# Performance work log

Hardware: AMD Instinct MI355X
Metric: run time of the kernel (lower is better)

## Reference

```python
import jax, jax.numpy as jnp
import numpy as np

B, D, N = 256, 128, 65536
P, K, P2 = 100, 4096, 10
T, MOM = 0.07, 0.5


def setup_inputs() -> dict:
    key = jax.random.key(0)
    k1, k2, k3, k4, k5 = jax.random.split(key, 5)
    stdv = 1.0 / np.sqrt(D / 3.0)
    memory_v1 = jax.random.uniform(k1, (N, D), minval=-stdv, maxval=stdv, dtype=jnp.float32)
    memory_v2 = jax.random.uniform(k2, (N, D), minval=-stdv, maxval=stdv, dtype=jnp.float32)
    v1 = jax.random.normal(k3, (B, D), dtype=jnp.float32)
    v2 = jax.random.normal(k4, (B, D), dtype=jnp.float32)
    y = jnp.arange(B, dtype=jnp.int32)  # unique sample ids in the bank
    idx = jax.random.randint(k5, (B, K + P), 0, N, dtype=jnp.int32)
    idx = idx.at[:, 0].set(y)  # first column is the ground-truth positive (as in torch)
    return {"epoch": 0, "v1": v1, "v2": v2, "y": y, "idx": idx,
            "memory_v1": memory_v1, "memory_v2": memory_v2}


def reference(epoch, v1, v2, y, idx, memory_v1, memory_v2):
    # --- gather contrastive keys from the memory banks (detached in torch) ---
    w1 = jax.lax.stop_gradient(memory_v1)[idx]  # [B, K+P, D]
    w2 = jax.lax.stop_gradient(memory_v2)[idx]  # [B, K+P, D]

    # similarity logits against the student feature v2
    out = jnp.exp(jnp.einsum('bkd,bd->bk', w1, v2) / T)  # [B, K+P]

    # --- hard positive selection via teacher/student relation gap ---
    t_rel = jnp.einsum('bkd,bd->bk',
                       w1 / jnp.linalg.norm(w1, axis=2, keepdims=True),
                       v1 / jnp.linalg.norm(v1, axis=1, keepdims=True))
    s_rel = jnp.einsum('bkd,bd->bk',
                       w2 / jnp.linalg.norm(w2, axis=2, keepdims=True),
                       v2 / jnp.linalg.norm(v2, axis=1, keepdims=True))
    diff = t_rel[:, :P] - s_rel[:, :P]            # [B, P]
    order = jnp.argsort(-diff, axis=1)            # descending sort ('hard' mode)
    sel = order[:, :P2].at[:, 0].set(0)           # force slot 0 = ground-truth positive

    out_pos = jnp.take_along_axis(out, sel, axis=1)  # [B, P2]
    out_neg = out[:, P:P + K]                        # [B, K]
    out_cat = jnp.concatenate([out_pos, out_neg], axis=1)  # [B, P2+K]

    # normalization constant Z (first-iteration estimate; a detached scalar in torch)
    Z = jax.lax.stop_gradient(out_cat.mean() * N)
    out_final = (out_cat / Z)[:, :, None]  # [B, P2+K, 1]

    # --- momentum memory update (no_grad in torch) ---
    l = memory_v1[y] * MOM + v1 * (1.0 - MOM)
    new_mem_v1 = memory_v1.at[y].set(l / jnp.linalg.norm(l, axis=1, keepdims=True))
    new_mem_v1 = jax.lax.stop_gradient(new_mem_v1)
    # (memory_v2 is updated identically in torch but not returned; omitted from outputs)

    return out_final, new_mem_v1
```

## Files before the change

### kernel.cpp

```cpp
#include <hip/hip_runtime.h>
#include <math.h>

constexpr int B_ = 256;
constexpr int D_ = 128;
constexpr int N_ = 65536;
constexpr int P_ = 100;
constexpr int K_ = 4096;
constexpr int P2_ = 10;
constexpr int KP_ = K_ + P_;
constexpr int OC_ = P2_ + K_;
constexpr int NBIN_ = 8;
constexpr int SLOT_ = 768;
constexpr int GCOPY_ = 2048;
constexpr int GGATH_ = B_ * NBIN_;
constexpr int GCOS_ = B_;
constexpr int NPART_ = GGATH_ + B_;
constexpr float T_ = 0.07f;

__global__ __launch_bounds__(256) void k_bin(
    const int* __restrict__ idx, unsigned* __restrict__ lists,
    int* __restrict__ counts)
{
  const int b = blockIdx.x;
  const int tid = threadIdx.x;
  __shared__ int cnt[NBIN_];
  if (tid < NBIN_) cnt[tid] = 0;
  __syncthreads();
  const int4* __restrict__ src = reinterpret_cast<const int4*>(idx + (size_t)b * KP_ + P_);
#pragma unroll
  for (int i = 0; i < 4; ++i) {
    const int4 r4 = src[i * 256 + tid];
    const int ks = (i * 256 + tid) * 4;
    const int rows[4] = {r4.x, r4.y, r4.z, r4.w};
#pragma unroll
    for (int u = 0; u < 4; ++u) {
      const int row = rows[u];
      const int bin = row >> 13;
      const int slot = atomicAdd(&cnt[bin], 1);
      if (slot < SLOT_)
        lists[((size_t)(b * NBIN_ + bin)) * SLOT_ + slot] =
            ((unsigned)(ks + u) << 16) | (unsigned)row;
    }
  }
  __syncthreads();
  if (tid < NBIN_) counts[b * NBIN_ + tid] = min(cnt[tid], SLOT_);
}

__global__ __launch_bounds__(256) void k_main(
    const float* __restrict__ v1, const float* __restrict__ v2,
    const int* __restrict__ idx, const float* __restrict__ mem1,
    const float* __restrict__ mem2, const unsigned* __restrict__ lists,
    const int* __restrict__ counts, float* __restrict__ out,
    float* __restrict__ outmem, double* __restrict__ wpart)
{
  const int tid = threadIdx.x;
  const unsigned bid = blockIdx.x;
  __shared__ double lacc[4];
  __shared__ float sbuf[2 * D_];
  __shared__ double sdiff[P_];
  __shared__ float swout[P_];

  if (bid < GCOPY_) {
    const int r = bid & 7, q = bid >> 3;
    const size_t base = ((size_t)r * 8192 + (size_t)q * 32) * D_;
    const float4* __restrict__ s = reinterpret_cast<const float4*>(mem1 + base);
    float4* __restrict__ d = reinterpret_cast<float4*>(outmem + base);
#pragma unroll
    for (int i = 0; i < 4; ++i) d[i * 256 + tid] = s[i * 256 + tid];
  } else if (bid < GCOPY_ + GGATH_) {
    const int g = bid - GCOPY_;
    const int bin = g & 7, b = g >> 3;
    const int count = counts[b * NBIN_ + bin];
    const unsigned* __restrict__ lb = lists + ((size_t)(b * NBIN_ + bin)) * SLOT_;
    const int j = tid & 7, gg = tid >> 3;
    const float4* __restrict__ v2p = reinterpret_cast<const float4*>(v2 + (size_t)b * D_);
    const float4 x0 = v2p[j], x1 = v2p[j + 8], x2 = v2p[j + 16], x3 = v2p[j + 24];
    float* __restrict__ outb = out + (size_t)b * OC_ + P2_;

    double de = 0.0;
    int s = gg;
    for (; s + 32 < count; s += 64) {
      const unsigned e0 = lb[s];
      const unsigned e1 = lb[s + 32];
      const float4* __restrict__ p0 = reinterpret_cast<const float4*>(mem1 + (size_t)(e0 & 0xFFFFu) * D_);
      const float4* __restrict__ p1 = reinterpret_cast<const float4*>(mem1 + (size_t)(e1 & 0xFFFFu) * D_);
      const float4 a0 = p0[j], a1 = p0[j + 8], a2 = p0[j + 16], a3 = p0[j + 24];
      const float4 b0 = p1[j], b1 = p1[j + 8], b2 = p1[j + 16], b3 = p1[j + 24];
      float s0 = a0.x * x0.x + a0.y * x0.y + a0.z * x0.z + a0.w * x0.w
               + a1.x * x1.x + a1.y * x1.y + a1.z * x1.z + a1.w * x1.w
               + a2.x * x2.x + a2.y * x2.y + a2.z * x2.z + a2.w * x2.w
               + a3.x * x3.x + a3.y * x3.y + a3.z * x3.z + a3.w * x3.w;
      float s1 = b0.x * x0.x + b0.y * x0.y + b0.z * x0.z + b0.w * x0.w
               + b1.x * x1.x + b1.y * x1.y + b1.z * x1.z + b1.w * x1.w
               + b2.x * x2.x + b2.y * x2.y + b2.z * x2.z + b2.w * x2.w
               + b3.x * x3.x + b3.y * x3.y + b3.z * x3.z + b3.w * x3.w;
#pragma unroll
      for (int sh = 1; sh < 8; sh <<= 1) {
        s0 += __shfl_xor(s0, sh);
        s1 += __shfl_xor(s1, sh);
      }
      if (j == 0) {
        const float e0f = expf(s0 * (1.0f / T_));
        const float e1f = expf(s1 * (1.0f / T_));
        outb[e0 >> 16] = e0f;
        outb[e1 >> 16] = e1f;
        de += (double)e0f + (double)e1f;
      }
    }
    for (; s < count; s += 32) {
      const unsigned e0 = lb[s];
      const float4* __restrict__ p0 = reinterpret_cast<const float4*>(mem1 + (size_t)(e0 & 0xFFFFu) * D_);
      const float4 a0 = p0[j], a1 = p0[j + 8], a2 = p0[j + 16], a3 = p0[j + 24];
      float s0 = a0.x * x0.x + a0.y * x0.y + a0.z * x0.z + a0.w * x0.w
               + a1.x * x1.x + a1.y * x1.y + a1.z * x1.z + a1.w * x1.w
               + a2.x * x2.x + a2.y * x2.y + a2.z * x2.z + a2.w * x2.w
               + a3.x * x3.x + a3.y * x3.y + a3.z * x3.z + a3.w * x3.w;
#pragma unroll
      for (int sh = 1; sh < 8; sh <<= 1) s0 += __shfl_xor(s0, sh);
      if (j == 0) {
        const float e0f = expf(s0 * (1.0f / T_));
        outb[e0 >> 16] = e0f;
        de += (double)e0f;
      }
    }
#pragma unroll
    for (int sh = 1; sh < 64; sh <<= 1) de += __shfl_xor(de, sh);
    if ((tid & 63) == 0) lacc[tid >> 6] = de;
    __syncthreads();
    if (tid == 0) wpart[g] = (lacc[0] + lacc[1]) + (lacc[2] + lacc[3]);
  } else {
    const int b = bid - GCOPY_ - GGATH_;
    if (tid < 32)
      reinterpret_cast<float4*>(sbuf)[tid] =
          reinterpret_cast<const float4*>(v2 + (size_t)b * D_)[tid];
    else if (tid < 64)
      reinterpret_cast<float4*>(sbuf)[tid] =
          reinterpret_cast<const float4*>(v1 + (size_t)b * D_)[tid - 32];
    __syncthreads();
    if (tid < P_) {
      double n2 = 0.0, n1 = 0.0;
#pragma unroll 8
      for (int jj = 0; jj < D_; ++jj) {
        n2 += (double)sbuf[jj] * sbuf[jj];
        n1 += (double)sbuf[D_ + jj] * sbuf[D_ + jj];
      }
      const double inv_n1 = 1.0 / sqrt(n1);
      const double inv_n2 = 1.0 / sqrt(n2);
      const int row = idx[(size_t)b * KP_ + tid];
      const float4* __restrict__ w1p = reinterpret_cast<const float4*>(mem1 + (size_t)row * D_);
      const float4* __restrict__ w2p = reinterpret_cast<const float4*>(mem2 + (size_t)row * D_);
      const float4* __restrict__ x2p = reinterpret_cast<const float4*>(sbuf);
      const float4* __restrict__ x1p = reinterpret_cast<const float4*>(sbuf + D_);
      double so = 0, sn1 = 0, st = 0, sn2 = 0, ss = 0;
#pragma unroll 4
      for (int jj = 0; jj < 32; ++jj) {
        const float4 a  = w1p[jj];
        const float4 cc = w2p[jj];
        const float4 y1 = x1p[jj];
        const float4 y2 = x2p[jj];
        so  += (double)a.x * y2.x + (double)a.y * y2.y + (double)a.z * y2.z + (double)a.w * y2.w;
        sn1 += (double)a.x * a.x  + (double)a.y * a.y  + (double)a.z * a.z  + (double)a.w * a.w;
        st  += (double)a.x * y1.x + (double)a.y * y1.y + (double)a.z * y1.z + (double)a.w * y1.w;
        sn2 += (double)cc.x * cc.x + (double)cc.y * cc.y + (double)cc.z * cc.z + (double)cc.w * cc.w;
        ss  += (double)cc.x * y2.x + (double)cc.y * y2.y + (double)cc.z * y2.z + (double)cc.w * y2.w;
      }
      const double t_rel = st * inv_n1 / sqrt(sn1);
      const double s_rel = ss * inv_n2 / sqrt(sn2);
      sdiff[tid] = t_rel - s_rel;
      swout[tid] = expf((float)(so * (1.0 / (double)T_)));
    }
    __syncthreads();
    if (tid < 64) {
      const int l = tid;
      const double va = sdiff[l];
      const double vb = (l < P_ - 64) ? sdiff[l + 64] : -1.0e300;
      bool ta = false, tb = (l >= P_ - 64);
      int sel[P2_];
#pragma unroll
      for (int t = 0; t < P2_; ++t) {
        double cv; int cj;
        const bool aok = !ta, bok = !tb;
        if (aok && (!bok || va >= vb)) { cv = va; cj = l; }
        else if (bok)                  { cv = vb; cj = l + 64; }
        else                           { cv = -1.0e300; cj = 0x7fffffff; }
#pragma unroll
        for (int sh = 1; sh < 64; sh <<= 1) {
          const double ov = __shfl_xor(cv, sh);
          const int    oj = __shfl_xor(cj, sh);
          if (ov > cv || (ov == cv && oj < cj)) { cv = ov; cj = oj; }
        }
        sel[t] = cj;
        if (cj == l) ta = true;
        if (cj == l + 64) tb = true;
      }
      if (l == 0) {
        sel[0] = 0;
        double sp = 0.0;
#pragma unroll
        for (int t = 0; t < P2_; ++t) {
          const float e = swout[sel[t]];
          out[(size_t)b * OC_ + t] = e;
          sp += (double)e;
        }
        wpart[GGATH_ + b] = sp;
      }
    }
  }
}

__global__ __launch_bounds__(256) void k_z(
    const double* __restrict__ wpart, float* __restrict__ invz)
{
  __shared__ double lds[4];
  const int tid = threadIdx.x;
  double s = 0.0;
  for (int i = tid; i < NPART_; i += 256) s += wpart[i];
#pragma unroll
  for (int sh = 1; sh < 64; sh <<= 1) s += __shfl_xor(s, sh);
  if ((tid & 63) == 0) lds[tid >> 6] = s;
  __syncthreads();
  if (tid == 0) {
    const double S = (lds[0] + lds[1]) + (lds[2] + lds[3]);
    const double Z = S / ((double)B_ * (double)OC_) * (double)N_;
    *invz = (float)(1.0 / Z);
  }
}

constexpr int NSC_ = (B_ * OC_ / 4 + 255) / 256;
__global__ __launch_bounds__(256) void k_scale_upd(
    float* __restrict__ out, const float* __restrict__ invz,
    const float* __restrict__ mem1, const float* __restrict__ v1,
    const int* __restrict__ y, float* __restrict__ dst)
{
  const int tid = threadIdx.x;
  if (blockIdx.x < NSC_) {
    const size_t i = (size_t)blockIdx.x * 256 + tid;
    constexpr size_t n4 = (size_t)B_ * OC_ / 4;
    if (i < n4) {
      const float sc = *invz;
      float4 v = reinterpret_cast<float4*>(out)[i];
      v.x *= sc; v.y *= sc; v.z *= sc; v.w *= sc;
      reinterpret_cast<float4*>(out)[i] = v;
    }
  } else if (tid < 64) {
    const int b = blockIdx.x - NSC_;
    const int lane = tid;
    const int row = y[b];
    const float2 m = *reinterpret_cast<const float2*>(mem1 + (size_t)row * D_ + lane * 2);
    const float2 a = *reinterpret_cast<const float2*>(v1 + (size_t)b * D_ + lane * 2);
    float2 l;
    l.x = m.x * 0.5f + a.x * 0.5f;
    l.y = m.y * 0.5f + a.y * 0.5f;
    float n = l.x * l.x + l.y * l.y;
#pragma unroll
    for (int sh = 1; sh < 64; sh <<= 1) n += __shfl_xor(n, sh);
    const float inv = 1.0f / sqrtf(n);
    float2 o;
    o.x = l.x * inv;
    o.y = l.y * inv;
    *reinterpret_cast<float2*>(dst + (size_t)row * D_ + lane * 2) = o;
  }
}

extern "C" void kernel_launch(void* const* d_in, const int* in_sizes, int n_in,
                              void* d_out, int out_size, void* d_ws, size_t ws_size,
                              hipStream_t stream) {
  const float* v1   = (const float*)d_in[1];
  const float* v2   = (const float*)d_in[2];
  const int*   y    = (const int*)d_in[3];
  const int*   idx  = (const int*)d_in[4];
  const float* mem1 = (const float*)d_in[5];
  const float* mem2 = (const float*)d_in[6];

  float* out    = (float*)d_out;
  float* outmem = out + (size_t)B_ * OC_;

  char* ws = (char*)d_ws;
  double*   wpart  = (double*)ws;
  int*      counts = (int*)(ws + 32768);
  unsigned* lists  = (unsigned*)(ws + 65536);
  float*    invz   = (float*)(ws + 65536 + (size_t)B_ * NBIN_ * SLOT_ * 4);

  k_bin<<<B_, 256, 0, stream>>>(idx, lists, counts);
  k_main<<<GCOPY_ + GGATH_ + GCOS_, 256, 0, stream>>>(
      v1, v2, idx, mem1, mem2, lists, counts, out, outmem, wpart);
  k_z<<<1, 256, 0, stream>>>(wpart, invz);
  k_scale_upd<<<NSC_ + B_, 256, 0, stream>>>(out, invz, mem1, v1, y, outmem);
}
```

Baseline: 73.74 us.

## Stage gathered logits in bin-order scratch and scatter via LDS in final kernel

```diff
diff --git a/kernel.cpp b/kernel.cpp
--- a/kernel.cpp
+++ b/kernel.cpp
@@ -11,9 +11,9 @@
 constexpr int OC_ = P2_ + K_;
 constexpr int NBIN_ = 8;
 constexpr int SLOT_ = 768;
+constexpr int GCOS_ = B_;
 constexpr int GCOPY_ = 2048;
 constexpr int GGATH_ = B_ * NBIN_;
-constexpr int GCOS_ = B_;
 constexpr int NPART_ = GGATH_ + B_;
 constexpr float T_ = 0.07f;
 
@@ -50,8 +50,9 @@
     const float* __restrict__ v1, const float* __restrict__ v2,
     const int* __restrict__ idx, const float* __restrict__ mem1,
     const float* __restrict__ mem2, const unsigned* __restrict__ lists,
-    const int* __restrict__ counts, float* __restrict__ out,
-    float* __restrict__ outmem, double* __restrict__ wpart)
+    const int* __restrict__ counts, float* __restrict__ evals,
+    float* __restrict__ wsel, float* __restrict__ outmem,
+    double* __restrict__ wpart)
 {
   const int tid = threadIdx.x;
   const unsigned bid = blockIdx.x;
@@ -59,33 +60,138 @@
   __shared__ float sbuf[2 * D_];
   __shared__ double sdiff[P_];
   __shared__ float swout[P_];
-
-  if (bid < GCOPY_) {
-    const int r = bid & 7, q = bid >> 3;
+  __shared__ double dsn2[P_], dss[P_];
+  __shared__ double dinv[2];
+
+  if (bid < GCOS_) {
+    const int b = bid;
+    if (tid < 32)
+      reinterpret_cast<float4*>(sbuf)[tid] =
+          reinterpret_cast<const float4*>(v2 + (size_t)b * D_)[tid];
+    else if (tid < 64)
+      reinterpret_cast<float4*>(sbuf)[tid] =
+          reinterpret_cast<const float4*>(v1 + (size_t)b * D_)[tid - 32];
+    __syncthreads();
+    if (tid < 64) {
+      const float2* s2 = reinterpret_cast<const float2*>(sbuf);
+      const float2 a = s2[tid];
+      const float2 c = s2[64 + tid];
+      double dn2 = (double)a.x * a.x + (double)a.y * a.y;
+      double dn1 = (double)c.x * c.x + (double)c.y * c.y;
+#pragma unroll
+      for (int sh = 1; sh < 64; sh <<= 1) {
+        dn2 += __shfl_xor(dn2, sh);
+        dn1 += __shfl_xor(dn1, sh);
+      }
+      if (tid == 0) { dinv[0] = 1.0 / sqrt(dn1); dinv[1] = 1.0 / sqrt(dn2); }
+    }
+    if (tid >= 128 && tid < 128 + P_) {
+      const int r = tid - 128;
+      const int row = idx[(size_t)b * KP_ + r];
+      const float4* __restrict__ w2p = reinterpret_cast<const float4*>(mem2 + (size_t)row * D_);
+      const float4* __restrict__ x2p = reinterpret_cast<const float4*>(sbuf);
+      double sn2 = 0, ss = 0;
+#pragma unroll 4
+      for (int jj = 0; jj < 32; ++jj) {
+        const float4 cc = w2p[jj];
+        const float4 y2 = x2p[jj];
+        sn2 += (double)cc.x * cc.x + (double)cc.y * cc.y + (double)cc.z * cc.z + (double)cc.w * cc.w;
+        ss  += (double)cc.x * y2.x + (double)cc.y * y2.y + (double)cc.z * y2.z + (double)cc.w * y2.w;
+      }
+      dsn2[r] = sn2; dss[r] = ss;
+    }
+    double so = 0, sn1 = 0, st = 0;
+    if (tid < P_) {
+      const int row = idx[(size_t)b * KP_ + tid];
+      const float4* __restrict__ w1p = reinterpret_cast<const float4*>(mem1 + (size_t)row * D_);
+      const float4* __restrict__ x2p = reinterpret_cast<const float4*>(sbuf);
+      const float4* __restrict__ x1p = reinterpret_cast<const float4*>(sbuf + D_);
+#pragma unroll 4
+      for (int jj = 0; jj < 32; ++jj) {
+        const float4 a  = w1p[jj];
+        const float4 y1 = x1p[jj];
+        const float4 y2 = x2p[jj];
+        so  += (double)a.x * y2.x + (double)a.y * y2.y + (double)a.z * y2.z + (double)a.w * y2.w;
+        sn1 += (double)a.x * a.x  + (double)a.y * a.y  + (double)a.z * a.z  + (double)a.w * a.w;
+        st  += (double)a.x * y1.x + (double)a.y * y1.y + (double)a.z * y1.z + (double)a.w * y1.w;
+      }
+    }
+    __syncthreads();
+    if (tid < P_) {
+      const double t_rel = st * dinv[0] / sqrt(sn1);
+      const double s_rel = dss[tid] * dinv[1] / sqrt(dsn2[tid]);
+      sdiff[tid] = t_rel - s_rel;
+      swout[tid] = expf((float)(so * (1.0 / (double)T_)));
+    }
+    __syncthreads();
+    if (tid < 64) {
+      const int l = tid;
+      const double va = sdiff[l];
+      const double vb = (l < P_ - 64) ? sdiff[l + 64] : -1.0e300;
+      bool ta = false, tb = (l >= P_ - 64);
+      int sel[P2_];
+#pragma unroll
+      for (int t = 0; t < P2_; ++t) {
+        double cv; int cj;
+        const bool aok = !ta, bok = !tb;
+        if (aok && (!bok || va >= vb)) { cv = va; cj = l; }
+        else if (bok)                  { cv = vb; cj = l + 64; }
+        else                           { cv = -1.0e300; cj = 0x7fffffff; }
+#pragma unroll
+        for (int sh = 1; sh < 64; sh <<= 1) {
+          const double ov = __shfl_xor(cv, sh);
+          const int    oj = __shfl_xor(cj, sh);
+          if (ov > cv || (ov == cv && oj < cj)) { cv = ov; cj = oj; }
+        }
+        sel[t] = cj;
+        if (cj == l) ta = true;
+        if (cj == l + 64) tb = true;
+      }
+      if (l == 0) {
+        sel[0] = 0;
+        double sp = 0.0;
+#pragma unroll
+        for (int t = 0; t < P2_; ++t) {
+          const float e = swout[sel[t]];
+          wsel[b * P2_ + t] = e;
+          sp += (double)e;
+        }
+        wpart[GGATH_ + b] = sp;
+      }
+    }
+  } else if (bid < GCOS_ + GCOPY_) {
+    const int g = bid - GCOS_;
+    const int r = g & 7, q = g >> 3;
     const size_t base = ((size_t)r * 8192 + (size_t)q * 32) * D_;
     const float4* __restrict__ s = reinterpret_cast<const float4*>(mem1 + base);
     float4* __restrict__ d = reinterpret_cast<float4*>(outmem + base);
 #pragma unroll
     for (int i = 0; i < 4; ++i) d[i * 256 + tid] = s[i * 256 + tid];
-  } else if (bid < GCOPY_ + GGATH_) {
-    const int g = bid - GCOPY_;
+  } else {
+    const int g = bid - GCOS_ - GCOPY_;
     const int bin = g & 7, b = g >> 3;
     const int count = counts[b * NBIN_ + bin];
     const unsigned* __restrict__ lb = lists + ((size_t)(b * NBIN_ + bin)) * SLOT_;
+    float* __restrict__ eb = evals + ((size_t)(b * NBIN_ + bin)) * SLOT_;
     const int j = tid & 7, gg = tid >> 3;
     const float4* __restrict__ v2p = reinterpret_cast<const float4*>(v2 + (size_t)b * D_);
     const float4 x0 = v2p[j], x1 = v2p[j + 8], x2 = v2p[j + 16], x3 = v2p[j + 24];
-    float* __restrict__ outb = out + (size_t)b * OC_ + P2_;
 
     double de = 0.0;
     int s = gg;
-    for (; s + 32 < count; s += 64) {
+    for (; s + 96 < count; s += 128) {
       const unsigned e0 = lb[s];
       const unsigned e1 = lb[s + 32];
+      const unsigned e2 = lb[s + 64];
+      const unsigned e3 = lb[s + 96];
       const float4* __restrict__ p0 = reinterpret_cast<const float4*>(mem1 + (size_t)(e0 & 0xFFFFu) * D_);
       const float4* __restrict__ p1 = reinterpret_cast<const float4*>(mem1 + (size_t)(e1 & 0xFFFFu) * D_);
+      const float4* __restrict__ p2 = reinterpret_cast<const float4*>(mem1 + (size_t)(e2 & 0xFFFFu) * D_);
+      const float4* __restrict__ p3 = reinterpret_cast<const float4*>(mem1 + (size_t)(e3 & 0xFFFFu) * D_);
       const float4 a0 = p0[j], a1 = p0[j + 8], a2 = p0[j + 16], a3 = p0[j + 24];
       const float4 b0 = p1[j], b1 = p1[j + 8], b2 = p1[j + 16], b3 = p1[j + 24];
+      const float4 c0 = p2[j], c1 = p2[j + 8], c2 = p2[j + 16], c3 = p2[j + 24];
+      const float4 d0 = p3[j], d1 = p3[j + 8], d2 = p3[j + 16], d3 = p3[j + 24];
       float s0 = a0.x * x0.x + a0.y * x0.y + a0.z * x0.z + a0.w * x0.w
                + a1.x * x1.x + a1.y * x1.y + a1.z * x1.z + a1.w * x1.w
                + a2.x * x2.x + a2.y * x2.y + a2.z * x2.z + a2.w * x2.w
@@ -94,17 +200,28 @@
                + b1.x * x1.x + b1.y * x1.y + b1.z * x1.z + b1.w * x1.w
                + b2.x * x2.x + b2.y * x2.y + b2.z * x2.z + b2.w * x2.w
                + b3.x * x3.x + b3.y * x3.y + b3.z * x3.z + b3.w * x3.w;
+      float s2v = c0.x * x0.x + c0.y * x0.y + c0.z * x0.z + c0.w * x0.w
+                + c1.x * x1.x + c1.y * x1.y + c1.z * x1.z + c1.w * x1.w
+                + c2.x * x2.x + c2.y * x2.y + c2.z * x2.z + c2.w * x2.w
+                + c3.x * x3.x + c3.y * x3.y + c3.z * x3.z + c3.w * x3.w;
+      float s3v = d0.x * x0.x + d0.y * x0.y + d0.z * x0.z + d0.w * x0.w
+                + d1.x * x1.x + d1.y * x1.y + d1.z * x1.z + d1.w * x1.w
+                + d2.x * x2.x + d2.y * x2.y + d2.z * x2.z + d2.w * x2.w
+                + d3.x * x3.x + d3.y * x3.y + d3.z * x3.z + d3.w * x3.w;
 #pragma unroll
       for (int sh = 1; sh < 8; sh <<= 1) {
         s0 += __shfl_xor(s0, sh);
         s1 += __shfl_xor(s1, sh);
+        s2v += __shfl_xor(s2v, sh);
+        s3v += __shfl_xor(s3v, sh);
       }
       if (j == 0) {
-        const float e0f = expf(s0 * (1.0f / T_));
-        const float e1f = expf(s1 * (1.0f / T_));
-        outb[e0 >> 16] = e0f;
-        outb[e1 >> 16] = e1f;
-        de += (double)e0f + (double)e1f;
+        const float f0 = expf(s0 * (1.0f / T_));
+        const float f1 = expf(s1 * (1.0f / T_));
+        const float f2 = expf(s2v * (1.0f / T_));
+        const float f3 = expf(s3v * (1.0f / T_));
+        eb[s] = f0; eb[s + 32] = f1; eb[s + 64] = f2; eb[s + 96] = f3;
+        de += ((double)f0 + (double)f1) + ((double)f2 + (double)f3);
       }
     }
     for (; s < count; s += 32) {
@@ -118,9 +235,9 @@
 #pragma unroll
       for (int sh = 1; sh < 8; sh <<= 1) s0 += __shfl_xor(s0, sh);
       if (j == 0) {
-        const float e0f = expf(s0 * (1.0f / T_));
-        outb[e0 >> 16] = e0f;
-        de += (double)e0f;
+        const float f0 = expf(s0 * (1.0f / T_));
+        eb[s] = f0;
+        de += (double)f0;
       }
     }
 #pragma unroll
@@ -128,83 +245,6 @@
     if ((tid & 63) == 0) lacc[tid >> 6] = de;
     __syncthreads();
     if (tid == 0) wpart[g] = (lacc[0] + lacc[1]) + (lacc[2] + lacc[3]);
-  } else {
-    const int b = bid - GCOPY_ - GGATH_;
-    if (tid < 32)
-      reinterpret_cast<float4*>(sbuf)[tid] =
-          reinterpret_cast<const float4*>(v2 + (size_t)b * D_)[tid];
-    else if (tid < 64)
-      reinterpret_cast<float4*>(sbuf)[tid] =
-          reinterpret_cast<const float4*>(v1 + (size_t)b * D_)[tid - 32];
-    __syncthreads();
-    if (tid < P_) {
-      double n2 = 0.0, n1 = 0.0;
-#pragma unroll 8
-      for (int jj = 0; jj < D_; ++jj) {
-        n2 += (double)sbuf[jj] * sbuf[jj];
-        n1 += (double)sbuf[D_ + jj] * sbuf[D_ + jj];
-      }
-      const double inv_n1 = 1.0 / sqrt(n1);
-      const double inv_n2 = 1.0 / sqrt(n2);
-      const int row = idx[(size_t)b * KP_ + tid];
-      const float4* __restrict__ w1p = reinterpret_cast<const float4*>(mem1 + (size_t)row * D_);
-      const float4* __restrict__ w2p = reinterpret_cast<const float4*>(mem2 + (size_t)row * D_);
-      const float4* __restrict__ x2p = reinterpret_cast<const float4*>(sbuf);
-      const float4* __restrict__ x1p = reinterpret_cast<const float4*>(sbuf + D_);
-      double so = 0, sn1 = 0, st = 0, sn2 = 0, ss = 0;
-#pragma unroll 4
-      for (int jj = 0; jj < 32; ++jj) {
-        const float4 a  = w1p[jj];
-        const float4 cc = w2p[jj];
-        const float4 y1 = x1p[jj];
-        const float4 y2 = x2p[jj];
-        so  += (double)a.x * y2.x + (double)a.y * y2.y + (double)a.z * y2.z + (double)a.w * y2.w;
-        sn1 += (double)a.x * a.x  + (double)a.y * a.y  + (double)a.z * a.z  + (double)a.w * a.w;
-        st  += (double)a.x * y1.x + (double)a.y * y1.y + (double)a.z * y1.z + (double)a.w * y1.w;
-        sn2 += (double)cc.x * cc.x + (double)cc.y * cc.y + (double)cc.z * cc.z + (double)cc.w * cc.w;
-        ss  += (double)cc.x * y2.x + (double)cc.y * y2.y + (double)cc.z * y2.z + (double)cc.w * y2.w;
-      }
-      const double t_rel = st * inv_n1 / sqrt(sn1);
-      const double s_rel = ss * inv_n2 / sqrt(sn2);
-      sdiff[tid] = t_rel - s_rel;
-      swout[tid] = expf((float)(so * (1.0 / (double)T_)));
-    }
-    __syncthreads();
-    if (tid < 64) {
-      const int l = tid;
-      const double va = sdiff[l];
-      const double vb = (l < P_ - 64) ? sdiff[l + 64] : -1.0e300;
-      bool ta = false, tb = (l >= P_ - 64);
-      int sel[P2_];
-#pragma unroll
-      for (int t = 0; t < P2_; ++t) {
-        double cv; int cj;
-        const bool aok = !ta, bok = !tb;
-        if (aok && (!bok || va >= vb)) { cv = va; cj = l; }
-        else if (bok)                  { cv = vb; cj = l + 64; }
-        else                           { cv = -1.0e300; cj = 0x7fffffff; }
-#pragma unroll
-        for (int sh = 1; sh < 64; sh <<= 1) {
-          const double ov = __shfl_xor(cv, sh);
-          const int    oj = __shfl_xor(cj, sh);
-          if (ov > cv || (ov == cv && oj < cj)) { cv = ov; cj = oj; }
-        }
-        sel[t] = cj;
-        if (cj == l) ta = true;
-        if (cj == l + 64) tb = true;
-      }
-      if (l == 0) {
-        sel[0] = 0;
-        double sp = 0.0;
-#pragma unroll
-        for (int t = 0; t < P2_; ++t) {
-          const float e = swout[sel[t]];
-          out[(size_t)b * OC_ + t] = e;
-          sp += (double)e;
-        }
-        wpart[GGATH_ + b] = sp;
-      }
-    }
   }
 }
 
@@ -226,28 +266,32 @@
   }
 }
 
-constexpr int NSC_ = (B_ * OC_ / 4 + 255) / 256;
-__global__ __launch_bounds__(256) void k_scale_upd(
-    float* __restrict__ out, const float* __restrict__ invz,
-    const float* __restrict__ mem1, const float* __restrict__ v1,
-    const int* __restrict__ y, float* __restrict__ dst)
+__global__ __launch_bounds__(256) void k_out(
+    const unsigned* __restrict__ lists, const int* __restrict__ counts,
+    const float* __restrict__ evals, const float* __restrict__ wsel,
+    const float* __restrict__ invz, const float* __restrict__ mem1,
+    const float* __restrict__ v1, const int* __restrict__ y,
+    float* __restrict__ out, float* __restrict__ outmem)
 {
+  __shared__ float srow[K_];
+  const int b = blockIdx.x;
   const int tid = threadIdx.x;
-  if (blockIdx.x < NSC_) {
-    const size_t i = (size_t)blockIdx.x * 256 + tid;
-    constexpr size_t n4 = (size_t)B_ * OC_ / 4;
-    if (i < n4) {
-      const float sc = *invz;
-      float4 v = reinterpret_cast<float4*>(out)[i];
-      v.x *= sc; v.y *= sc; v.z *= sc; v.w *= sc;
-      reinterpret_cast<float4*>(out)[i] = v;
-    }
-  } else if (tid < 64) {
-    const int b = blockIdx.x - NSC_;
-    const int lane = tid;
+  const float sc = *invz;
+#pragma unroll
+  for (int bin = 0; bin < NBIN_; ++bin) {
+    const int cnt = counts[b * NBIN_ + bin];
+    const unsigned* __restrict__ lb = lists + ((size_t)(b * NBIN_ + bin)) * SLOT_;
+    const float* __restrict__ eb = evals + ((size_t)(b * NBIN_ + bin)) * SLOT_;
+    for (int s = tid; s < cnt; s += 256) srow[lb[s] >> 16] = eb[s];
+  }
+  __syncthreads();
+  float* __restrict__ orow = out + (size_t)b * OC_;
+  if (tid < P2_) orow[tid] = wsel[b * P2_ + tid] * sc;
+  for (int i = tid; i < K_; i += 256) orow[P2_ + i] = srow[i] * sc;
+  if (tid < 64) {
     const int row = y[b];
-    const float2 m = *reinterpret_cast<const float2*>(mem1 + (size_t)row * D_ + lane * 2);
-    const float2 a = *reinterpret_cast<const float2*>(v1 + (size_t)b * D_ + lane * 2);
+    const float2 m = *reinterpret_cast<const float2*>(mem1 + (size_t)row * D_ + tid * 2);
+    const float2 a = *reinterpret_cast<const float2*>(v1 + (size_t)b * D_ + tid * 2);
     float2 l;
     l.x = m.x * 0.5f + a.x * 0.5f;
     l.y = m.y * 0.5f + a.y * 0.5f;
@@ -258,7 +302,7 @@
     float2 o;
     o.x = l.x * inv;
     o.y = l.y * inv;
-    *reinterpret_cast<float2*>(dst + (size_t)row * D_ + lane * 2) = o;
+    *reinterpret_cast<float2*>(outmem + (size_t)row * D_ + tid * 2) = o;
   }
 }
 
@@ -276,14 +320,18 @@
   float* outmem = out + (size_t)B_ * OC_;
 
   char* ws = (char*)d_ws;
+  constexpr size_t LSZ = (size_t)B_ * NBIN_ * SLOT_ * 4;
   double*   wpart  = (double*)ws;
   int*      counts = (int*)(ws + 32768);
   unsigned* lists  = (unsigned*)(ws + 65536);
-  float*    invz   = (float*)(ws + 65536 + (size_t)B_ * NBIN_ * SLOT_ * 4);
+  float*    evals  = (float*)(ws + 65536 + LSZ);
+  float*    wsel   = (float*)(ws + 65536 + 2 * LSZ);
+  float*    invz   = (float*)(ws + 65536 + 2 * LSZ + 16384);
 
   k_bin<<<B_, 256, 0, stream>>>(idx, lists, counts);
-  k_main<<<GCOPY_ + GGATH_ + GCOS_, 256, 0, stream>>>(
-      v1, v2, idx, mem1, mem2, lists, counts, out, outmem, wpart);
+  k_main<<<GCOS_ + GCOPY_ + GGATH_, 256, 0, stream>>>(
+      v1, v2, idx, mem1, mem2, lists, counts, evals, wsel, outmem, wpart);
   k_z<<<1, 256, 0, stream>>>(wpart, invz);
-  k_scale_upd<<<NSC_ + B_, 256, 0, stream>>>(out, invz, mem1, v1, y, outmem);
-}
+  k_out<<<B_, 256, 0, stream>>>(lists, counts, evals, wsel, invz,
+                                mem1, v1, y, out, outmem);
+}
```

Result: faster. 65.99 us (-10.5%).
